# Optimization experiments

Hardware: AMD Instinct MI355X
Metric: run time of the kernel (lower is better)

Reference implementation:

```python
import jax, jax.numpy as jnp
import numpy as np

HEAD_DIM = 128
N_HEADS = 16
N_KV_HEADS = 4
THETA = 10000.0
EPS = 1e-6


def setup_inputs() -> dict:
    key = jax.random.key(0)
    k1, k2, k3 = jax.random.split(key, 3)
    B, S = 2, 2048
    xq = jax.random.normal(k1, (B, S, N_HEADS * HEAD_DIM), dtype=jnp.float32)
    xk = jax.random.normal(k2, (B, S, N_KV_HEADS * HEAD_DIM), dtype=jnp.float32)
    xv = jax.random.normal(k3, (B, S, N_KV_HEADS * HEAD_DIM), dtype=jnp.float32)
    return {"xq": xq, "xk": xk, "xv": xv}


def _rope(x):
    # x: [b, h, s, d]; half-split rotary (y1 = x1*cos + x2*sin, y2 = -x1*sin + x2*cos)
    d = x.shape[-1]
    s = x.shape[2]
    inv_freq = (1.0 / THETA) ** (jnp.arange(0, d, 2, dtype=jnp.float32) / d)
    t = jnp.arange(s, dtype=jnp.float32)
    freqs = t[:, None] * inv_freq[None, :]          # [s, d/2]
    cos = jnp.cos(freqs)[None, None]                 # [1,1,s,d/2]
    sin = jnp.sin(freqs)[None, None]
    x1, x2 = jnp.split(x, 2, axis=-1)
    y1 = x1 * cos + x2 * sin
    y2 = -x1 * sin + x2 * cos
    return jnp.concatenate([y1, y2], axis=-1).astype(x.dtype)


def reference(xq, xk, xv):
    B, S, _ = xq.shape
    # b s (h a) -> b h s a
    q = xq.reshape(B, S, N_HEADS, HEAD_DIM).transpose(0, 2, 1, 3)
    k = xk.reshape(B, S, N_KV_HEADS, HEAD_DIM).transpose(0, 2, 1, 3)
    v = xv.reshape(B, S, N_KV_HEADS, HEAD_DIM).transpose(0, 2, 1, 3)
    # qk-norm (L2 normalize last dim with eps clamp, like F.normalize)
    q = q / jnp.maximum(jnp.linalg.norm(q, axis=-1, keepdims=True), EPS)
    k = k / jnp.maximum(jnp.linalg.norm(k, axis=-1, keepdims=True), EPS)
    # RoPE
    q = _rope(q)
    k = _rope(k)
    # GQA: repeat kv heads to match q heads
    rep = N_HEADS // N_KV_HEADS
    k = jnp.repeat(k, rep, axis=1)
    v = jnp.repeat(v, rep, axis=1)
    scale = 1.0 / jnp.sqrt(jnp.asarray(HEAD_DIM, dtype=q.dtype))
    scores = jnp.einsum('bhqd,bhkd->bhqk', q, k) * scale
    causal = jnp.tril(jnp.ones((S, S), dtype=bool))
    scores = jnp.where(causal[None, None], scores, jnp.asarray(-jnp.inf, scores.dtype))
    probs = jax.nn.softmax(scores, axis=-1)
    out = jnp.einsum('bhqk,bhkd->bhqd', probs, v)
    # b h s a -> b s (h a)
    return out.transpose(0, 2, 1, 3).reshape(B, S, N_HEADS * HEAD_DIM)
```

## Files before the change

### kernel.cpp

```cpp
#include <hip/hip_runtime.h>
#include <hip/hip_bf16.h>
#include <stdint.h>

#define S_LEN 2048
#define NB    2
#define HQ    16
#define HKV   4
#define HD    128
#define KVB   64
#define QBW   32
#define QBB   128

typedef __bf16 bf16_t;
typedef __attribute__((ext_vector_type(8)))  __bf16 bf16x8;
typedef __attribute__((ext_vector_type(4)))  float  f32x4;
typedef __attribute__((ext_vector_type(16))) float  f32x16;
typedef __attribute__((ext_vector_type(4)))  unsigned int u32x4;

__constant__ int kOrder24[24] = {7,22,23,20,21, 6,18,19,16,17, 5,14,15,12,13,
                                 4,10,11,8,9, 3, 2, 1, 0};

__device__ __forceinline__ void gload_lds16(const bf16_t* g, bf16_t* l) {
  __builtin_amdgcn_global_load_lds(
      (const __attribute__((address_space(1))) unsigned int*)g,
      (__attribute__((address_space(3))) unsigned int*)l, 16, 0, 0);
}
__device__ __forceinline__ uint32_t pack2(float lo, float hi) {
  uint32_t a = (uint32_t)__builtin_bit_cast(unsigned short, (bf16_t)lo);
  uint32_t b = (uint32_t)__builtin_bit_cast(unsigned short, (bf16_t)hi);
  return a | (b << 16);
}

__global__ void qk_preproc_kernel(const float* __restrict__ xq,
                                  const float* __restrict__ xk,
                                  bf16_t* __restrict__ Qr,
                                  bf16_t* __restrict__ Kf) {
  int wid  = (blockIdx.x * blockDim.x + threadIdx.x) >> 6;
  int lane = threadIdx.x & 63;
  const int per_bs = HQ + HKV;
  int b   = wid / (S_LEN * per_bs);
  int rem = wid - b * (S_LEN * per_bs);
  int s   = rem / per_bs;
  int hh  = rem - s * per_bs;
  const float* src;
  float scale;
  if (hh < HQ) {
    src = xq + ((size_t)(b * S_LEN + s) * (HQ * HD)) + hh * HD;
    scale = 0.08838834764831845f * 1.4426950408889634f;
  } else {
    src = xk + ((size_t)(b * S_LEN + s) * (HKV * HD)) + (hh - HQ) * HD;
    scale = 1.0f;
  }
  float x1 = src[lane];
  float x2 = src[64 + lane];
  float ss = x1 * x1 + x2 * x2;
  #pragma unroll
  for (int m = 1; m < 64; m <<= 1) ss += __shfl_xor(ss, m, 64);
  float rinv = scale / fmaxf(sqrtf(ss), 1e-6f);
  float inv = exp2f(-(float)lane * 0.20762050593046938f);
  float ang = (float)s * inv;
  float cs = cosf(ang), sn = sinf(ang);
  float q1 = x1 * rinv, q2 = x2 * rinv;
  bf16_t y1 = (bf16_t)(q1 * cs + q2 * sn);
  bf16_t y2 = (bf16_t)(q2 * cs - q1 * sn);
  if (hh < HQ) {
    bf16_t* dst = Qr + (((size_t)(b * HQ + hh) * S_LEN + s) * HD);
    dst[lane]      = y1;
    dst[64 + lane] = y2;
  } else {
    bf16_t* dst = Kf + ((size_t)((b * HKV + (hh - HQ)) * 32 + (s >> 6))) * (KVB * HD);
    const int sl = s & 63, half = sl >> 5, r0k = sl & 31;
    const int kk = lane >> 4, hi = (lane >> 3) & 1, pos = lane & 7;
    const int a1 = (kk * 128 + half * 64 + hi * 32 + r0k) * 8 + pos;
    dst[a1]        = y1;
    dst[a1 + 4096] = y2;
  }
}

__global__ void v_preproc_kernel(const float* __restrict__ xv,
                                 bf16_t* __restrict__ Vf) {
  __shared__ bf16_t tile[HD][34];
  const int bid = blockIdx.x;
  const int bh  = bid >> 6;
  const int r6  = bid & 63;
  const int sc  = r6 >> 1;
  const int j   = r6 & 1;
  const int b = bh >> 2, hh = bh & 3;
  const int d  = threadIdx.x & 127;
  const int s2 = threadIdx.x >> 7;
  const float* src = xv + (size_t)b * S_LEN * (HKV * HD) + hh * HD;
  #pragma unroll 4
  for (int it = 0; it < 16; ++it) {
    int sl = it * 2 + s2;
    int s  = sc * 64 + j * 32 + sl;
    tile[d][sl] = (bf16_t)src[(size_t)s * (HKV * HD) + d];
  }
  __syncthreads();
  bf16_t* dstb = Vf + ((size_t)bh * 32 + sc) * (HD * KVB);
  const int dd   = threadIdx.x >> 1;
  const int dt   = dd >> 5, r0v = dd & 31;
  #pragma unroll
  for (int i = 0; i < 2; ++i) {
    const int cl = (threadIdx.x & 1) * 2 + i;
    const int c  = j * 4 + cl;
    const int n  = (c >> 1) * 256 + dt * 64 + (c & 1) * 32 + r0v;
    *reinterpret_cast<bf16x8*>(dstb + n * 8) =
        *reinterpret_cast<const bf16x8*>(&tile[dd][cl * 8]);
  }
}

__global__ __launch_bounds__(256, 3)
void attn_kernel(const bf16_t* __restrict__ Qr,
                 const bf16_t* __restrict__ Kf,
                 const bf16_t* __restrict__ Vf,
                 float* __restrict__ out,
                 float* __restrict__ Opart,
                 float2* __restrict__ mlpart,
                 int split, int upb) {
  __shared__ bf16_t Kb[2][KVB * HD];
  __shared__ bf16_t Vb[HD * KVB];

  const int w    = threadIdx.x >> 6;
  const int lane = threadIdx.x & 63;
  const int r0   = lane & 31;
  const int hi   = lane >> 5;

  const int lid = (int)blockIdx.x;
  const int p   = lid & 7;
  const int qq  = lid >> 3;
  const int j   = qq & 3;
  const int k   = qq >> 2;
  const int b   = p >> 2;
  const int kvh = p & 3;
  const int h   = kvh * 4 + j;
  const int bh  = b * 16 + h;
  const int u   = split ? kOrder24[k] : (15 - k);
  int qt, t0, t1;
  if (!split || u < 8) {
    qt = u; t0 = 0; t1 = 2 * qt + 2;
  } else {
    int v = u - 8;
    qt = 8 + (v >> 1);
    int T = 2 * qt + 2, mid = qt + 1;
    if (v & 1) { t0 = mid; t1 = T; } else { t0 = 0; t1 = mid; }
  }
  const bool full = (t0 == 0) && (t1 == 2 * qt + 2);
  const int qw0  = qt * QBB + w * QBW;
  const int qrow = qw0 + r0;
  const int qmax = qw0 + 31;

  const bf16_t* Qbase = Qr + (size_t)(b * HQ  + h  ) * S_LEN * HD;
  const bf16_t* Kbase = Kf + (size_t)(b * HKV + kvh) * 32 * (KVB * HD);
  const bf16_t* Vbase = Vf + (size_t)(b * HKV + kvh) * 32 * (HD * KVB);

  const int soff = (w * 256 + lane) * 8;

  bf16x8 qf[8];
  #pragma unroll
  for (int kk = 0; kk < 8; ++kk)
    qf[kk] = *reinterpret_cast<const bf16x8*>(Qbase + (size_t)qrow * HD + kk * 16 + hi * 8);

  f32x16 accO[4];
  #pragma unroll
  for (int dt = 0; dt < 4; ++dt)
    #pragma unroll
    for (int e = 0; e < 16; ++e) accO[dt][e] = 0.f;
  float m = -3.0e38f, l = 0.f;

  {
    const bf16_t* kg = Kbase + (size_t)t0 * (KVB * HD);
    #pragma unroll
    for (int i = 0; i < 4; ++i)
      gload_lds16(kg + soff + i * 512, &Kb[0][soff + i * 512]);
  }

  for (int t = t0; t < t1; ++t) {
    const int pb = (t - t0) & 1;
    __builtin_amdgcn_s_barrier();
    {
      const bf16_t* vg = Vbase + (size_t)t * (HD * KVB);
      #pragma unroll
      for (int i = 0; i < 4; ++i)
        gload_lds16(vg + soff + i * 512, &Vb[soff + i * 512]);
      const int tn = (t + 1 < t1) ? t + 1 : t;
      const bf16_t* kg = Kbase + (size_t)tn * (KVB * HD);
      #pragma unroll
      for (int i = 0; i < 4; ++i)
        gload_lds16(kg + soff + i * 512, &Kb[pb ^ 1][soff + i * 512]);
    }
    asm volatile("s_waitcnt vmcnt(8)" ::: "memory");
    __builtin_amdgcn_sched_barrier(0);
    __builtin_amdgcn_s_barrier();
    __builtin_amdgcn_sched_barrier(0);

    const int kv0 = t * KVB;
    const bool active = (kv0 <= qmax);
    float p2[32];
    u32x4 pw[4];
    if (active) {
      const bf16_t* kb = &Kb[pb][0];
      f32x16 st0, st1;
      #pragma unroll
      for (int e = 0; e < 16; ++e) { st0[e] = 0.f; st1[e] = 0.f; }
      __builtin_amdgcn_s_setprio(1);
      #pragma unroll
      for (int kk = 0; kk < 8; ++kk) {
        bf16x8 k0 = *reinterpret_cast<const bf16x8*>(kb + kk * 1024 + lane * 8);
        bf16x8 k1 = *reinterpret_cast<const bf16x8*>(kb + kk * 1024 + 512 + lane * 8);
        st0 = __builtin_amdgcn_mfma_f32_32x32x16_bf16(k0, qf[kk], st0, 0, 0, 0);
        st1 = __builtin_amdgcn_mfma_f32_32x32x16_bf16(k1, qf[kk], st1, 0, 0, 0);
      }
      __builtin_amdgcn_s_setprio(0);

      const bool need_mask = (kv0 + 63 > qw0);
      #pragma unroll
      for (int jj = 0; jj < 2; ++jj)
        #pragma unroll
        for (int e = 0; e < 16; ++e) {
          float s = jj ? st1[e] : st0[e];
          if (need_mask) {
            int kv = kv0 + jj * 32 + (e & 3) + 8 * (e >> 2) + 4 * hi;
            s = (kv > qrow) ? -3.0e38f : s;
          }
          p2[jj * 16 + e] = s;
        }
      float mt[16];
      #pragma unroll
      for (int e = 0; e < 16; ++e) mt[e] = fmaxf(p2[e], p2[e + 16]);
      #pragma unroll
      for (int e = 0; e < 8; ++e) mt[e] = fmaxf(mt[e], mt[e + 8]);
      #pragma unroll
      for (int e = 0; e < 4; ++e) mt[e] = fmaxf(mt[e], mt[e + 4]);
      float lmx = fmaxf(fmaxf(mt[0], mt[1]), fmaxf(mt[2], mt[3]));
      float cmx = fmaxf(lmx, __shfl_xor(lmx, 32, 64));
      if (!__all(cmx <= m + 8.0f)) {
        float mnew = fmaxf(m, cmx);
        float resc = __builtin_amdgcn_exp2f(m - mnew);
        m = mnew;
        l *= resc;
        #pragma unroll
        for (int dt = 0; dt < 4; ++dt)
          #pragma unroll
          for (int e = 0; e < 16; ++e) accO[dt][e] *= resc;
      }
      #pragma unroll
      for (int e = 0; e < 32; ++e) p2[e] = __builtin_amdgcn_exp2f(p2[e] - m);
      float sv[16];
      #pragma unroll
      for (int e = 0; e < 16; ++e) sv[e] = p2[e] + p2[e + 16];
      #pragma unroll
      for (int e = 0; e < 8; ++e) sv[e] += sv[e + 8];
      #pragma unroll
      for (int e = 0; e < 4; ++e) sv[e] += sv[e + 4];
      float lsum = (sv[0] + sv[1]) + (sv[2] + sv[3]);
      l += lsum + __shfl_xor(lsum, 32, 64);

      #pragma unroll
      for (int jj = 0; jj < 2; ++jj) {
        const int o = jj * 16;
        {
          uint32_t A = pack2(p2[o + 0], p2[o + 1]);
          uint32_t C = pack2(p2[o + 2], p2[o + 3]);
          uint32_t B = pack2(p2[o + 4], p2[o + 5]);
          uint32_t D = pack2(p2[o + 6], p2[o + 7]);
          uint32_t At = __shfl_xor(A, 32, 64), Ct = __shfl_xor(C, 32, 64);
          uint32_t Bt = __shfl_xor(B, 32, 64), Dt = __shfl_xor(D, 32, 64);
          pw[2 * jj] = hi ? (u32x4){Bt, Dt, B, D} : (u32x4){A, C, At, Ct};
        }
        {
          uint32_t A = pack2(p2[o + 8],  p2[o + 9]);
          uint32_t C = pack2(p2[o + 10], p2[o + 11]);
          uint32_t B = pack2(p2[o + 12], p2[o + 13]);
          uint32_t D = pack2(p2[o + 14], p2[o + 15]);
          uint32_t At = __shfl_xor(A, 32, 64), Ct = __shfl_xor(C, 32, 64);
          uint32_t Bt = __shfl_xor(B, 32, 64), Dt = __shfl_xor(D, 32, 64);
          pw[2 * jj + 1] = hi ? (u32x4){Bt, Dt, B, D} : (u32x4){A, C, At, Ct};
        }
      }
    }

    asm volatile("s_waitcnt vmcnt(4)" ::: "memory");
    __builtin_amdgcn_sched_barrier(0);
    __builtin_amdgcn_s_barrier();
    __builtin_amdgcn_sched_barrier(0);

    if (active) {
      const bf16_t* vb = &Vb[0];
      __builtin_amdgcn_s_setprio(1);
      #pragma unroll
      for (int kk = 0; kk < 4; ++kk) {
        bf16x8 pf = __builtin_bit_cast(bf16x8, pw[kk]);
        #pragma unroll
        for (int dt = 0; dt < 4; ++dt) {
          bf16x8 vf = *reinterpret_cast<const bf16x8*>(vb + kk * 2048 + dt * 512 + lane * 8);
          accO[dt] = __builtin_amdgcn_mfma_f32_32x32x16_bf16(vf, pf, accO[dt], 0, 0, 0);
        }
      }
      __builtin_amdgcn_s_setprio(0);
    }
  }

  if (full) {
    const float inv = 1.0f / l;
    float* orow = out + ((size_t)(b * S_LEN + qrow) * (HQ * HD)) + h * HD + hi * 4;
    #pragma unroll
    for (int dt = 0; dt < 4; ++dt)
      #pragma unroll
      for (int rg = 0; rg < 4; ++rg) {
        f32x4 v4 = { accO[dt][4 * rg + 0] * inv, accO[dt][4 * rg + 1] * inv,
                     accO[dt][4 * rg + 2] * inv, accO[dt][4 * rg + 3] * inv };
        *reinterpret_cast<f32x4*>(orow + dt * 32 + rg * 8) = v4;
      }
  } else {
    const int c    = (t0 != 0) ? 1 : 0;
    const int pidx = ((bh << 3) + (qt - 8)) * 2 + c;
    float* Op = Opart + (size_t)pidx * (QBB * HD) + (size_t)(w * QBW + r0) * HD + hi * 4;
    #pragma unroll
    for (int dt = 0; dt < 4; ++dt)
      #pragma unroll
      for (int rg = 0; rg < 4; ++rg) {
        f32x4 v4 = { accO[dt][4 * rg + 0], accO[dt][4 * rg + 1],
                     accO[dt][4 * rg + 2], accO[dt][4 * rg + 3] };
        *reinterpret_cast<f32x4*>(Op + dt * 32 + rg * 8) = v4;
      }
    if (!hi) mlpart[(size_t)pidx * QBB + w * QBW + r0] = make_float2(m, l);
  }
}

__global__ void combine_kernel(const float* __restrict__ Opart,
                               const float2* __restrict__ mlpart,
                               float* __restrict__ out) {
  const int j  = blockIdx.x;
  const int bh = j >> 3;
  const int qt = 8 + (j & 7);
  const int b  = bh >> 4;
  const int h  = bh & 15;
  const int r  = threadIdx.x >> 1;
  const int d0 = (threadIdx.x & 1) * 64;
  const size_t p0 = (size_t)(j * 2)     * (QBB * HD) + (size_t)r * HD + d0;
  const size_t p1 = (size_t)(j * 2 + 1) * (QBB * HD) + (size_t)r * HD + d0;
  const float2 ml0 = mlpart[(size_t)(j * 2)     * QBB + r];
  const float2 ml1 = mlpart[(size_t)(j * 2 + 1) * QBB + r];
  const float M  = fmaxf(ml0.x, ml1.x);
  float a0 = exp2f(ml0.x - M), a1 = exp2f(ml1.x - M);
  const float inv = 1.0f / (a0 * ml0.y + a1 * ml1.y);
  a0 *= inv; a1 *= inv;
  const int qrow = qt * QBB + r;
  float* orow = out + ((size_t)(b * S_LEN + qrow) * (HQ * HD)) + h * HD + d0;
  #pragma unroll
  for (int i = 0; i < 16; ++i) {
    f32x4 o0 = *reinterpret_cast<const f32x4*>(Opart + p0 + i * 4);
    f32x4 o1 = *reinterpret_cast<const f32x4*>(Opart + p1 + i * 4);
    f32x4 res = { a0 * o0[0] + a1 * o1[0], a0 * o0[1] + a1 * o1[1],
                  a0 * o0[2] + a1 * o1[2], a0 * o0[3] + a1 * o1[3] };
    *reinterpret_cast<f32x4*>(orow + i * 4) = res;
  }
}

extern "C" void kernel_launch(void* const* d_in, const int* in_sizes, int n_in,
                              void* d_out, int out_size, void* d_ws, size_t ws_size,
                              hipStream_t stream) {
  const float* xq = (const float*)d_in[0];
  const float* xk = (const float*)d_in[1];
  const float* xv = (const float*)d_in[2];
  float* out = (float*)d_out;

  char* ws = (char*)d_ws;
  size_t off = 0;
  bf16_t* Qr = (bf16_t*)(ws + off); off += (size_t)NB * HQ  * S_LEN * HD * sizeof(bf16_t);
  bf16_t* Kf = (bf16_t*)(ws + off); off += (size_t)NB * HKV * S_LEN * HD * sizeof(bf16_t);
  bf16_t* Vf = (bf16_t*)(ws + off); off += (size_t)NB * HKV * S_LEN * HD * sizeof(bf16_t);
  float*  Opart  = (float*)(ws + off);  off += (size_t)512 * QBB * HD * sizeof(float);
  float2* mlpart = (float2*)(ws + off); off += (size_t)512 * QBB * sizeof(float2);
  const int split = (ws_size >= off) ? 1 : 0;
  const int upb   = split ? 24 : 16;

  const int nrow = NB * S_LEN * (HQ + HKV);
  qk_preproc_kernel<<<nrow / 4, 256, 0, stream>>>(xq, xk, Qr, Kf);

  v_preproc_kernel<<<NB * HKV * 64, 256, 0, stream>>>(xv, Vf);

  attn_kernel<<<32 * upb, 256, 0, stream>>>(Qr, Kf, Vf, out, Opart, mlpart,
                                            split, upb);
  if (split)
    combine_kernel<<<256, 256, 0, stream>>>(Opart, mlpart, out);
}
```

Measured before the change: 100.4 us.

## Fuse split-KV combine into attention kernel via last-block atomic counter

Removes the separate combine kernel launch. Each split block writes its partial output and running max/sum stats, then bumps a per-tile atomic counter, and the second block to arrive merges both partials into the output. A memset of the flags buffer is added before the preprocessing kernels. Separately, the RoPE sin/cos calls switch to the fast intrinsics, which trades some accuracy at large angles for cheaper math.

```diff
diff --git a/kernel.cpp b/kernel.cpp
--- a/kernel.cpp
+++ b/kernel.cpp
@@ -59,7 +59,7 @@
   float rinv = scale / fmaxf(sqrtf(ss), 1e-6f);
   float inv = exp2f(-(float)lane * 0.20762050593046938f);
   float ang = (float)s * inv;
-  float cs = cosf(ang), sn = sinf(ang);
+  float cs = __cosf(ang), sn = __sinf(ang);
   float q1 = x1 * rinv, q2 = x2 * rinv;
   bf16_t y1 = (bf16_t)(q1 * cs + q2 * sn);
   bf16_t y2 = (bf16_t)(q2 * cs - q1 * sn);
@@ -116,9 +116,11 @@
                  float* __restrict__ out,
                  float* __restrict__ Opart,
                  float2* __restrict__ mlpart,
+                 int* __restrict__ flags,
                  int split, int upb) {
   __shared__ bf16_t Kb[2][KVB * HD];
   __shared__ bf16_t Vb[HD * KVB];
+  __shared__ int sh_last;
 
   const int w    = threadIdx.x >> 6;
   const int lane = threadIdx.x & 63;
@@ -313,7 +315,8 @@
       }
   } else {
     const int c    = (t0 != 0) ? 1 : 0;
-    const int pidx = ((bh << 3) + (qt - 8)) * 2 + c;
+    const int j2   = (bh << 3) + (qt - 8);
+    const int pidx = j2 * 2 + c;
     float* Op = Opart + (size_t)pidx * (QBB * HD) + (size_t)(w * QBW + r0) * HD + hi * 4;
     #pragma unroll
     for (int dt = 0; dt < 4; ++dt)
@@ -324,36 +327,35 @@
         *reinterpret_cast<f32x4*>(Op + dt * 32 + rg * 8) = v4;
       }
     if (!hi) mlpart[(size_t)pidx * QBB + w * QBW + r0] = make_float2(m, l);
-  }
-}
-
-__global__ void combine_kernel(const float* __restrict__ Opart,
-                               const float2* __restrict__ mlpart,
-                               float* __restrict__ out) {
-  const int j  = blockIdx.x;
-  const int bh = j >> 3;
-  const int qt = 8 + (j & 7);
-  const int b  = bh >> 4;
-  const int h  = bh & 15;
-  const int r  = threadIdx.x >> 1;
-  const int d0 = (threadIdx.x & 1) * 64;
-  const size_t p0 = (size_t)(j * 2)     * (QBB * HD) + (size_t)r * HD + d0;
-  const size_t p1 = (size_t)(j * 2 + 1) * (QBB * HD) + (size_t)r * HD + d0;
-  const float2 ml0 = mlpart[(size_t)(j * 2)     * QBB + r];
-  const float2 ml1 = mlpart[(size_t)(j * 2 + 1) * QBB + r];
-  const float M  = fmaxf(ml0.x, ml1.x);
-  float a0 = exp2f(ml0.x - M), a1 = exp2f(ml1.x - M);
-  const float inv = 1.0f / (a0 * ml0.y + a1 * ml1.y);
-  a0 *= inv; a1 *= inv;
-  const int qrow = qt * QBB + r;
-  float* orow = out + ((size_t)(b * S_LEN + qrow) * (HQ * HD)) + h * HD + d0;
-  #pragma unroll
-  for (int i = 0; i < 16; ++i) {
-    f32x4 o0 = *reinterpret_cast<const f32x4*>(Opart + p0 + i * 4);
-    f32x4 o1 = *reinterpret_cast<const f32x4*>(Opart + p1 + i * 4);
-    f32x4 res = { a0 * o0[0] + a1 * o1[0], a0 * o0[1] + a1 * o1[1],
-                  a0 * o0[2] + a1 * o1[2], a0 * o0[3] + a1 * o1[3] };
-    *reinterpret_cast<f32x4*>(orow + i * 4) = res;
+
+    __threadfence();
+    __syncthreads();
+    if (threadIdx.x == 0)
+      sh_last = (atomicAdd(&flags[j2], 1) == 1) ? 1 : 0;
+    __syncthreads();
+    if (sh_last) {
+      __threadfence();
+      const int rr = threadIdx.x >> 1;
+      const int d0 = (threadIdx.x & 1) * 64;
+      const size_t pj0 = (size_t)(j2 * 2)     * (QBB * HD) + (size_t)rr * HD + d0;
+      const size_t pj1 = (size_t)(j2 * 2 + 1) * (QBB * HD) + (size_t)rr * HD + d0;
+      const float2 ml0 = mlpart[(size_t)(j2 * 2)     * QBB + rr];
+      const float2 ml1 = mlpart[(size_t)(j2 * 2 + 1) * QBB + rr];
+      const float M  = fmaxf(ml0.x, ml1.x);
+      float a0 = exp2f(ml0.x - M), a1 = exp2f(ml1.x - M);
+      const float invl = 1.0f / (a0 * ml0.y + a1 * ml1.y);
+      a0 *= invl; a1 *= invl;
+      const int qr2 = qt * QBB + rr;
+      float* orow = out + ((size_t)(b * S_LEN + qr2) * (HQ * HD)) + h * HD + d0;
+      #pragma unroll
+      for (int i = 0; i < 16; ++i) {
+        f32x4 o0 = *reinterpret_cast<const f32x4*>(Opart + pj0 + i * 4);
+        f32x4 o1 = *reinterpret_cast<const f32x4*>(Opart + pj1 + i * 4);
+        f32x4 res = { a0 * o0[0] + a1 * o1[0], a0 * o0[1] + a1 * o1[1],
+                      a0 * o0[2] + a1 * o1[2], a0 * o0[3] + a1 * o1[3] };
+        *reinterpret_cast<f32x4*>(orow + i * 4) = res;
+      }
+    }
   }
 }
 
@@ -372,16 +374,18 @@
   bf16_t* Vf = (bf16_t*)(ws + off); off += (size_t)NB * HKV * S_LEN * HD * sizeof(bf16_t);
   float*  Opart  = (float*)(ws + off);  off += (size_t)512 * QBB * HD * sizeof(float);
   float2* mlpart = (float2*)(ws + off); off += (size_t)512 * QBB * sizeof(float2);
+  int*    flags  = (int*)(ws + off);    off += 256 * sizeof(int);
   const int split = (ws_size >= off) ? 1 : 0;
   const int upb   = split ? 24 : 16;
 
+  if (split)
+    hipMemsetAsync(flags, 0, 256 * sizeof(int), stream);
+
   const int nrow = NB * S_LEN * (HQ + HKV);
   qk_preproc_kernel<<<nrow / 4, 256, 0, stream>>>(xq, xk, Qr, Kf);
 
   v_preproc_kernel<<<NB * HKV * 64, 256, 0, stream>>>(xv, Vf);
 
   attn_kernel<<<32 * upb, 256, 0, stream>>>(Qr, Kf, Vf, out, Opart, mlpart,
-                                            split, upb);
-  if (split)
-    combine_kernel<<<256, 256, 0, stream>>>(Opart, mlpart, out);
-}
+                                            flags, split, upb);
+}
```

New measurement: 222.5 us. 2.22x slower.
